# Performance work log

Measured on AMD Instinct MI355X. Metric: run time of the kernel, lower is better.

The kernel has to match this reference:

```python
import jax, jax.numpy as jnp
import numpy as np

B, T, H, W = 2, 4, 32, 32
DINO_DIM, COG_DIM, NUM_HEADS = 768, 1920, 12
HEAD_DIM = DINO_DIM // NUM_HEADS


def _layernorm(x, g, b, eps=1e-5):
    mu = jnp.mean(x, axis=-1, keepdims=True)
    var = jnp.mean(jnp.square(x - mu), axis=-1, keepdims=True)
    return (x - mu) * jax.lax.rsqrt(var + eps) * g + b


def setup_inputs() -> dict:
    key = jax.random.key(0)
    ks = jax.random.split(key, 12)
    s_d = 1.0 / np.sqrt(DINO_DIM)
    s_c = 1.0 / np.sqrt(COG_DIM)
    return {
        "dino_query": jax.random.normal(ks[0], (B, DINO_DIM, H, W), jnp.float32),
        "cogvideo_keys": jax.random.normal(ks[1], (B, T, H, W, COG_DIM), jnp.float32),
        "temporal_weights": jax.random.uniform(ks[2], (T,), jnp.float32),
        "Wq": jax.random.normal(ks[3], (DINO_DIM, DINO_DIM), jnp.float32) * s_d,
        "bq": jnp.zeros((DINO_DIM,), jnp.float32),
        "Wk": jax.random.normal(ks[4], (COG_DIM, DINO_DIM), jnp.float32) * s_c,
        "bk": jnp.zeros((DINO_DIM,), jnp.float32),
        "Wv": jax.random.normal(ks[5], (COG_DIM, DINO_DIM), jnp.float32) * s_c,
        "bv": jnp.zeros((DINO_DIM,), jnp.float32),
        "Wo": jax.random.normal(ks[6], (DINO_DIM, DINO_DIM), jnp.float32) * s_d,
        "bo": jnp.zeros((DINO_DIM,), jnp.float32),
        "gq": jnp.ones((DINO_DIM,), jnp.float32),
        "Bq": jnp.zeros((DINO_DIM,), jnp.float32),
        "gkv": jnp.ones((COG_DIM,), jnp.float32),
        "Bkv": jnp.zeros((COG_DIM,), jnp.float32),
    }


def reference(dino_query, cogvideo_keys, temporal_weights,
              Wq, bq, Wk, bk, Wv, bv, Wo, bo, gq, Bq, gkv, Bkv):
    b, c, h, w = dino_query.shape
    t = cogvideo_keys.shape[1]
    hw, tkv = h * w, t * cogvideo_keys.shape[2] * cogvideo_keys.shape[3]

    # [B,C,H,W] -> [B,H,W,C]; project after LayerNorm
    xq = _layernorm(jnp.transpose(dino_query, (0, 2, 3, 1)), gq, Bq)
    xkv = _layernorm(cogvideo_keys, gkv, Bkv)
    q = xq @ Wq + bq                      # [B,H,W,C]
    k = xkv @ Wk + bk                     # [B,T,Hk,Wk,C]
    v = xkv @ Wv + bv

    q = q.reshape(b, hw, NUM_HEADS, HEAD_DIM).transpose(0, 2, 1, 3)    # [B,nh,HW,hd]
    k = k.reshape(b, tkv, NUM_HEADS, HEAD_DIM).transpose(0, 2, 1, 3)   # [B,nh,TKV,hd]
    v = v.reshape(b, tkv, NUM_HEADS, HEAD_DIM).transpose(0, 2, 1, 3)

    scores = jnp.einsum('bnqd,bnkd->bnqk', q, k) / np.sqrt(HEAD_DIM)   # [B,nh,HW,TKV]
    # per-key temporal weight: each of the T frames contributes HW keys
    w_key = jnp.repeat(temporal_weights, tkv // t)                     # [TKV]
    scores = scores * w_key[None, None, None, :]
    probs = jax.nn.softmax(scores, axis=-1)

    out = jnp.einsum('bnqk,bnkd->bnqd', probs, v)                      # [B,nh,HW,hd]
    out = out.transpose(0, 2, 1, 3).reshape(b, h, w, c)
    out = out @ Wo + bo
    return jnp.transpose(out, (0, 3, 1, 2))                            # [B,C,H,W]
```

## Files before the change

### kernel.cpp

```cpp
#include <hip/hip_runtime.h>
#include <hip/hip_bf16.h>
#include <math.h>

#define BB   2
#define HWl  1024
#define DINO 768
#define COG  1920
#define NHh  12
#define TKV  4096
#define MQ   (BB*HWl)
#define MKV  (BB*TKV)
#define NSPL 4
#define ROWS_PER_SPLIT (BB*NHh*HWl)

typedef __attribute__((ext_vector_type(8))) short bf16x8;
typedef __attribute__((ext_vector_type(4))) float f32x4;

__device__ __forceinline__ unsigned short f2bf_bits(float f) {
    __hip_bfloat16 h = __float2bfloat16(f);
    return *reinterpret_cast<unsigned short*>(&h);
}

__device__ __forceinline__ void glds16(const __hip_bfloat16* g, __hip_bfloat16* l) {
    __builtin_amdgcn_global_load_lds((const __attribute__((address_space(1))) void*)g,
                                     (__attribute__((address_space(3))) void*)l, 16, 0, 0);
}

__global__ __launch_bounds__(256) void prep1(const float* __restrict__ dino,
                                             const float* __restrict__ cog,
                                             const float* __restrict__ gkv, const float* __restrict__ Bkv,
                                             const float* __restrict__ Wq, const float* __restrict__ Wk,
                                             const float* __restrict__ Wv, const float* __restrict__ Wo,
                                             float* __restrict__ xqT,
                                             __hip_bfloat16* __restrict__ xkv,
                                             __hip_bfloat16* WqT, __hip_bfloat16* WkvT, __hip_bfloat16* WoT) {
    int bid = blockIdx.x, tid = threadIdx.x;
    if (bid < 2048) {
        const int W = COG, W4 = W >> 2, NC = 8;
        int row = bid * 4 + (tid >> 6), lane = tid & 63;
        const float4* xr = (const float4*)(cog + (size_t)row * W);
        const float4* g4 = (const float4*)gkv;
        const float4* b4 = (const float4*)Bkv;
        float4 v[NC];
        float s = 0.f, ss = 0.f;
        #pragma unroll
        for (int i = 0; i < NC; ++i) {
            int c = lane + i * 64;
            float4 t = (c < W4) ? xr[c] : (float4){0.f, 0.f, 0.f, 0.f};
            v[i] = t;
            s  += t.x + t.y + t.z + t.w;
            ss += t.x * t.x + t.y * t.y + t.z * t.z + t.w * t.w;
        }
        #pragma unroll
        for (int off = 1; off < 64; off <<= 1) {
            s  += __shfl_xor(s, off);
            ss += __shfl_xor(ss, off);
        }
        float mu = s / W;
        float rstd = rsqrtf(ss / W - mu * mu + 1e-5f);
        ushort4* yr = (ushort4*)(xkv + (size_t)row * W);
        #pragma unroll
        for (int i = 0; i < NC; ++i) {
            int c = lane + i * 64;
            if (c < W4) {
                float4 t = v[i];
                float4 gg = g4[c], bb = b4[c];
                ushort4 o;
                o.x = f2bf_bits((t.x - mu) * rstd * gg.x + bb.x);
                o.y = f2bf_bits((t.y - mu) * rstd * gg.y + bb.y);
                o.z = f2bf_bits((t.z - mu) * rstd * gg.z + bb.z);
                o.w = f2bf_bits((t.w - mu) * rstd * gg.w + bb.w);
                yr[c] = o;
            }
        }
    } else if (bid < 2432) {
        int t = bid - 2048;
        int h0 = (t & 15) * 64;
        int c0 = ((t >> 4) % 12) * 64;
        int b = t / 192;
        __shared__ float T[64][65];
        #pragma unroll
        for (int i = 0; i < 16; ++i) {
            int idx = tid + i * 256;
            int c = idx >> 6, h = idx & 63;
            T[c][h] = dino[((size_t)b * DINO + c0 + c) * HWl + h0 + h];
        }
        __syncthreads();
        #pragma unroll
        for (int i = 0; i < 16; ++i) {
            int idx = tid + i * 256;
            int r = idx >> 6, c = idx & 63;
            xqT[((size_t)b * HWl + h0 + r) * DINO + c0 + c] = T[c][r];
        }
    } else {
        int bid2 = bid - 2432;
        int mid = bid2 / 1440, r = bid2 % 1440;
        int k0 = (r % 60) * 32, n0 = (r / 60) * 32;
        const float* src = (mid == 0) ? Wq : (mid == 1) ? Wk : (mid == 2) ? Wv : Wo;
        __hip_bfloat16* dst;
        int rowoff = 0;
        if (mid == 0) dst = WqT;
        else if (mid == 1) dst = WkvT;
        else if (mid == 2) { dst = WkvT; rowoff = 768; }
        else dst = WoT;
        int K = (mid == 1 || mid == 2) ? COG : DINO;
        if (k0 >= K) return;
        __shared__ float T[32][33];
        #pragma unroll
        for (int i = 0; i < 4; ++i) {
            int idx = tid + i * 256;
            int rr = idx >> 5, c = idx & 31;
            T[rr][c] = src[(size_t)(k0 + rr) * DINO + n0 + c];
        }
        __syncthreads();
        #pragma unroll
        for (int i = 0; i < 4; ++i) {
            int idx = tid + i * 256;
            int rr = idx >> 5, c = idx & 31;
            dst[(size_t)(rowoff + n0 + rr) * K + k0 + c] = __float2bfloat16(T[c][rr]);
        }
    }
}

__global__ __launch_bounds__(256) void prep2(const float* __restrict__ x,
                                             const float* __restrict__ g,
                                             const float* __restrict__ be,
                                             __hip_bfloat16* __restrict__ y) {
    const int W = DINO, NC = 3;
    int row = blockIdx.x * 4 + (threadIdx.x >> 6);
    int lane = threadIdx.x & 63;
    const float4* xr = (const float4*)(x + (size_t)row * W);
    const float4* g4 = (const float4*)g;
    const float4* b4 = (const float4*)be;
    float4 v[NC];
    float s = 0.f, ss = 0.f;
    #pragma unroll
    for (int i = 0; i < NC; ++i) {
        int c = lane + i * 64;
        float4 t = xr[c];
        v[i] = t;
        s  += t.x + t.y + t.z + t.w;
        ss += t.x * t.x + t.y * t.y + t.z * t.z + t.w * t.w;
    }
    #pragma unroll
    for (int off = 1; off < 64; off <<= 1) {
        s  += __shfl_xor(s, off);
        ss += __shfl_xor(ss, off);
    }
    float mu = s / W;
    float rstd = rsqrtf(ss / W - mu * mu + 1e-5f);
    ushort4* yr = (ushort4*)(y + (size_t)row * W);
    #pragma unroll
    for (int i = 0; i < NC; ++i) {
        int c = lane + i * 64;
        float4 t = v[i];
        float4 gg = g4[c], bb = b4[c];
        ushort4 o;
        o.x = f2bf_bits((t.x - mu) * rstd * gg.x + bb.x);
        o.y = f2bf_bits((t.y - mu) * rstd * gg.y + bb.y);
        o.z = f2bf_bits((t.z - mu) * rstd * gg.z + bb.z);
        o.w = f2bf_bits((t.w - mu) * rstd * gg.w + bb.w);
        yr[c] = o;
    }
}

#define VM4 asm volatile("s_waitcnt vmcnt(4)" ::: "memory")
#define VM2 asm volatile("s_waitcnt vmcnt(2)" ::: "memory")
#define VM0 asm volatile("s_waitcnt vmcnt(0)" ::: "memory")

#define STAGE_A(d, h, tau) do { \
    int _o = (aRow + (h) * 64) * Kd + (tau) * 64 + cgo; \
    __hip_bfloat16* _dp = SM + (d) * 32768 + (h) * 8192 + wido; \
    glds16(Ag + _o, _dp); \
    glds16(Ag + _o + 128 * Kd, _dp + 4096); \
} while (0)

#define STAGE_B(d, h, tau) do { \
    int _o = (bRow + (h) * 32) * Kd + (tau) * 64 + cgo; \
    __hip_bfloat16* _dp = SM + (d) * 32768 + 16384 + (h) * 8192 + wido; \
    glds16(Bg + _o, _dp); \
    glds16(Bg + _o + 128 * Kd, _dp + 4096); \
} while (0)

#define LDS_A_FRAG(dst, MH) do { \
    const __hip_bfloat16* _Ab = SM + cur * 32768 + (MH) * 8192 + aoff; \
    _Pragma("unroll") \
    for (int i = 0; i < 4; ++i) { \
        dst[i][0] = *(const bf16x8*)(_Ab + i * 1024 + c0); \
        dst[i][1] = *(const bf16x8*)(_Ab + i * 1024 + c1); \
    } \
} while (0)

#define LDS_B_FRAG(dst, NH) do { \
    const __hip_bfloat16* _Bb = SM + cur * 32768 + 16384 + (NH) * 8192 + boff; \
    _Pragma("unroll") \
    for (int j = 0; j < 2; ++j) { \
        dst[j][0] = *(const bf16x8*)(_Bb + j * 1024 + c0); \
        dst[j][1] = *(const bf16x8*)(_Bb + j * 1024 + c1); \
    } \
} while (0)

#define BARRIER_MFMA(MH, NH, af, bf) do { \
    __builtin_amdgcn_sched_barrier(0); \
    __builtin_amdgcn_s_barrier(); \
    __builtin_amdgcn_sched_barrier(0); \
    __builtin_amdgcn_s_setprio(1); \
    _Pragma("unroll") \
    for (int i = 0; i < 4; ++i) \
        _Pragma("unroll") \
        for (int j = 0; j < 2; ++j) { \
            f32x4 _t = acc[(MH) * 4 + i][(NH) * 2 + j]; \
            _t = __builtin_amdgcn_mfma_f32_16x16x32_bf16(af[i][0], bf[j][0], _t, 0, 0, 0); \
            _t = __builtin_amdgcn_mfma_f32_16x16x32_bf16(af[i][1], bf[j][1], _t, 0, 0, 0); \
            acc[(MH) * 4 + i][(NH) * 2 + j] = _t; \
        } \
    __builtin_amdgcn_s_setprio(0); \
    __builtin_amdgcn_sched_barrier(0); \
} while (0)

__global__ __launch_bounds__(512, 2) void stage1(const __hip_bfloat16* __restrict__ xq,
                                                 const __hip_bfloat16* __restrict__ WqT,
                                                 const float* __restrict__ bq,
                                                 __hip_bfloat16* __restrict__ qb,
                                                 const __hip_bfloat16* __restrict__ xkv,
                                                 const __hip_bfloat16* __restrict__ WkvT,
                                                 const float* __restrict__ bk,
                                                 const float* __restrict__ bv,
                                                 __hip_bfloat16* __restrict__ kb,
                                                 __hip_bfloat16* __restrict__ VT) {
    __shared__ __hip_bfloat16 SM[65536];
    int bid = blockIdx.x;
    int tid = threadIdx.x;
    int wid = tid >> 6, lane = tid & 63;
    int l4 = lane & 15, lq = lane >> 4;
    int wr = wid >> 2, wc = wid & 3;
    int tr = tid >> 3;
    int cgo = ((tid & 7) ^ (tr & 7)) * 8;
    int wido = wid * 512;

    const __hip_bfloat16 *Ag, *Bg;
    int m0, n0, Kd, NT, isQ;
    if (bid < 192) {
        m0 = (bid & 31) * 256; n0 = (bid >> 5) * 256;
        Ag = xkv; Bg = WkvT; Kd = COG; NT = COG / 64; isQ = 0;
    } else {
        int t = bid - 192;
        m0 = (t & 7) * 256; n0 = (t >> 3) * 256;
        Ag = xq; Bg = WqT; Kd = DINO; NT = DINO / 64; isQ = 1;
    }

    const int aRow = m0 + tr;
    const int bRow = n0 + ((tid >> 8) << 6) + (tr & 31);
    const int aoff = (wr * 64 + l4) * 64;
    const int boff = (wc * 32 + l4) * 64;
    const int c0 = ((lq) ^ (l4 & 7)) * 8;
    const int c1 = ((4 + lq) ^ (l4 & 7)) * 8;

    f32x4 acc[8][4];
    #pragma unroll
    for (int i = 0; i < 8; ++i)
        #pragma unroll
        for (int j = 0; j < 4; ++j) acc[i][j] = (f32x4){0.f, 0.f, 0.f, 0.f};

    bf16x8 a0[4][2], a1[4][2], b0[2][2], b1[2][2];

    STAGE_A(0, 0, 0); STAGE_B(0, 0, 0); STAGE_B(0, 1, 0); STAGE_A(0, 1, 0);
    VM0;
    __builtin_amdgcn_s_barrier();

    for (int g = 0; g < NT; ++g) {
        int cur = g & 1, nxt = cur ^ 1;
        bool s1 = (g + 1 < NT);
        LDS_A_FRAG(a0, 0);
        LDS_B_FRAG(b0, 0);
        if (s1) { STAGE_A(nxt, 0, g + 1); VM4; } else { VM2; }
        BARRIER_MFMA(0, 0, a0, b0);
        LDS_B_FRAG(b1, 1);
        if (s1) { STAGE_B(nxt, 0, g + 1); VM4; } else { VM0; }
        BARRIER_MFMA(0, 1, a0, b1);
        LDS_A_FRAG(a1, 1);
        if (s1) { STAGE_B(nxt, 1, g + 1); }
        BARRIER_MFMA(1, 1, a1, b1);
        if (s1) { STAGE_A(nxt, 1, g + 1); VM4; }
        BARRIER_MFMA(1, 0, a1, b0);
    }

    if (isQ) {
        #pragma unroll
        for (int ii = 0; ii < 8; ++ii)
            #pragma unroll
            for (int jj = 0; jj < 4; ++jj) {
                int m = m0 + wr * 128 + (ii >> 2) * 64 + (ii & 3) * 16 + lq * 4;
                int n = n0 + wc * 64 + (jj >> 1) * 32 + (jj & 1) * 16 + l4;
                float bb = bq[n];
                #pragma unroll
                for (int r = 0; r < 4; ++r)
                    qb[(size_t)(m + r) * DINO + n] = __float2bfloat16(acc[ii][jj][r] + bb);
            }
    } else if (n0 < 768) {
        #pragma unroll
        for (int ii = 0; ii < 8; ++ii)
            #pragma unroll
            for (int jj = 0; jj < 4; ++jj) {
                int m = m0 + wr * 128 + (ii >> 2) * 64 + (ii & 3) * 16 + lq * 4;
                int n = n0 + wc * 64 + (jj >> 1) * 32 + (jj & 1) * 16 + l4;
                float bb = bk[n];
                #pragma unroll
                for (int r = 0; r < 4; ++r)
                    kb[(size_t)(m + r) * DINO + n] = __float2bfloat16(acc[ii][jj][r] + bb);
            }
    } else {
        #pragma unroll
        for (int ii = 0; ii < 8; ++ii)
            #pragma unroll
            for (int jj = 0; jj < 4; ++jj) {
                int m = m0 + wr * 128 + (ii >> 2) * 64 + (ii & 3) * 16 + lq * 4;
                int nv = n0 - 768 + wc * 64 + (jj >> 1) * 32 + (jj & 1) * 16 + l4;
                float bb = bv[nv];
                #pragma unroll
                for (int r = 0; r < 4; ++r) {
                    int mm = m + r;
                    VT[((size_t)((mm >> 12) * 768 + nv)) * TKV + (mm & 4095)] =
                        __float2bfloat16(acc[ii][jj][r] + bb);
                }
            }
    }
}

__global__ __launch_bounds__(256) void gemm_o(const __hip_bfloat16* __restrict__ A,
                                              const __hip_bfloat16* __restrict__ Bt,
                                              const float* __restrict__ bias,
                                              float* __restrict__ out) {
    const int K = DINO;
    __shared__ __hip_bfloat16 As[64 * 64];
    __shared__ __hip_bfloat16 Bs[64 * 64];
    int m0 = blockIdx.x * 64, n0 = blockIdx.y * 64;
    int tid = threadIdx.x, w = tid >> 6, lane = tid & 63;
    int l4 = lane & 15, lq = lane >> 4;
    int mq = (w & 1) * 32, nq = (w >> 1) * 32;
    f32x4 acc[2][2];
    #pragma unroll
    for (int i = 0; i < 2; ++i)
        #pragma unroll
        for (int j = 0; j < 2; ++j) acc[i][j] = (f32x4){0.f, 0.f, 0.f, 0.f};

    int rr = tid >> 3;
    int gc = (tid & 7) ^ (rr & 7);
    const __hip_bfloat16* ag = A  + (size_t)(m0 + rr) * K + gc * 8;
    const __hip_bfloat16* bg = Bt + (size_t)(n0 + rr) * K + gc * 8;
    __hip_bfloat16* asl = As + (w * 8) * 64;
    __hip_bfloat16* bsl = Bs + (w * 8) * 64;
    int sws = l4 & 7;

    for (int k0 = 0; k0 < K; k0 += 64) {
        __syncthreads();
        #pragma unroll
        for (int g = 0; g < 2; ++g) {
            glds16(ag + (size_t)(g * 32) * K + k0, asl + g * 32 * 64);
            glds16(bg + (size_t)(g * 32) * K + k0, bsl + g * 32 * 64);
        }
        __syncthreads();
        #pragma unroll
        for (int h = 0; h < 2; ++h) {
            bf16x8 a[2], b[2];
            #pragma unroll
            for (int i = 0; i < 2; ++i)
                a[i] = *(const bf16x8*)(As + (mq + 16 * i + l4) * 64 + (((h * 4 + lq) ^ sws) * 8));
            #pragma unroll
            for (int j = 0; j < 2; ++j)
                b[j] = *(const bf16x8*)(Bs + (nq + 16 * j + l4) * 64 + (((h * 4 + lq) ^ sws) * 8));
            #pragma unroll
            for (int i = 0; i < 2; ++i)
                #pragma unroll
                for (int j = 0; j < 2; ++j)
                    acc[i][j] = __builtin_amdgcn_mfma_f32_16x16x32_bf16(b[j], a[i], acc[i][j], 0, 0, 0);
        }
    }
    #pragma unroll
    for (int i = 0; i < 2; ++i)
        #pragma unroll
        for (int j = 0; j < 2; ++j)
            #pragma unroll
            for (int r = 0; r < 4; ++r) {
                int n = n0 + nq + 16 * j + lq * 4 + r;
                int m = m0 + mq + 16 * i + l4;
                int b = m >> 10, hw = m & 1023;
                out[((size_t)b * DINO + n) * HWl + hw] = acc[i][j][r] + bias[n];
            }
}

__global__ __launch_bounds__(256) void attn4(const __hip_bfloat16* __restrict__ qb,
                                             const __hip_bfloat16* __restrict__ kb,
                                             const __hip_bfloat16* __restrict__ VT,
                                             const float* __restrict__ tw,
                                             __hip_bfloat16* __restrict__ Opart,
                                             float* __restrict__ lpart) {
    int bid = blockIdx.x;
    int g = bid % 96, qc = bid / 96;
    int s = g & 3, bh = g >> 2;
    int head = bh % NHh, b = bh / NHh;
    int tid = threadIdx.x, w = tid >> 6, lane = tid & 63;
    int l4 = lane & 15, lq = lane >> 4;

    __shared__ __hip_bfloat16 Ks[2 * 64 * 64];
    __shared__ __hip_bfloat16 Vs[2 * 64 * 64];
    __shared__ __hip_bfloat16 Ps[4 * 32 * 64];

    const __hip_bfloat16* qbase = qb + (size_t)(b * HWl + qc * 128 + w * 32 + l4) * DINO + head * 64;
    bf16x8 qA0 = *(const bf16x8*)(qbase + lq * 8);
    bf16x8 qA1 = *(const bf16x8*)(qbase + 32 + lq * 8);
    const __hip_bfloat16* qbase2 = qbase + (size_t)16 * DINO;
    bf16x8 qB0 = *(const bf16x8*)(qbase2 + lq * 8);
    bf16x8 qB1 = *(const bf16x8*)(qbase2 + 32 + lq * 8);

    float c = tw[s] * 0.125f * 1.44269504f;
    float l_iA = 0.f, l_iB = 0.f;
    f32x4 oA[4], oB[4];
    #pragma unroll
    for (int j = 0; j < 4; ++j) { oA[j] = (f32x4){0.f,0.f,0.f,0.f}; oB[j] = (f32x4){0.f,0.f,0.f,0.f}; }

    int rowA = w * 16 + (lane >> 3);
    int cg = (lane & 7) ^ ((lane >> 3) & 7);
    const __hip_bfloat16* kg0 = kb + (size_t)(b * TKV + s * 1024 + rowA) * DINO + head * 64 + cg * 8;
    const __hip_bfloat16* kg1 = kg0 + (size_t)8 * DINO;
    const __hip_bfloat16* vg0 = VT + (size_t)(b * 768 + head * 64 + rowA) * TKV + s * 1024 + cg * 8;
    const __hip_bfloat16* vg1 = vg0 + (size_t)8 * TKV;
    int klo0 = (w * 2 + 0) * 512, klo1 = (w * 2 + 1) * 512;

    int sw0 = (lq ^ (l4 & 7)) * 8;
    int sw1 = ((4 + lq) ^ (l4 & 7)) * 8;
    __hip_bfloat16* PsA = Ps + w * 2048 + l4 * 64;
    __hip_bfloat16* PsB = Ps + w * 2048 + (16 + l4) * 64;

    glds16(kg0, Ks + klo0);
    glds16(kg1, Ks + klo1);
    glds16(vg0, Vs + klo0);
    glds16(vg1, Vs + klo1);

    for (int kt = 0; kt < 16; ++kt) {
        int cur = (kt & 1) * 4096;
        __syncthreads();
        if (kt < 15) {
            int nxt = cur ^ 4096;
            glds16(kg0 + (size_t)(kt + 1) * 64 * DINO, Ks + nxt + klo0);
            glds16(kg1 + (size_t)(kt + 1) * 64 * DINO, Ks + nxt + klo1);
            glds16(vg0 + (kt + 1) * 64, Vs + nxt + klo0);
            glds16(vg1 + (kt + 1) * 64, Vs + nxt + klo1);
        }
        const __hip_bfloat16* Kc = Ks + cur;
        const __hip_bfloat16* Vc = Vs + cur;

        f32x4 stA[4], stB[4];
        #pragma unroll
        for (int j = 0; j < 4; ++j) {
            const __hip_bfloat16* kr = Kc + (16 * j + l4) * 64;
            bf16x8 kf0 = *(const bf16x8*)(kr + sw0);
            bf16x8 kf1 = *(const bf16x8*)(kr + sw1);
            f32x4 a = (f32x4){0.f,0.f,0.f,0.f};
            a = __builtin_amdgcn_mfma_f32_16x16x32_bf16(kf0, qA0, a, 0, 0, 0);
            a = __builtin_amdgcn_mfma_f32_16x16x32_bf16(kf1, qA1, a, 0, 0, 0);
            stA[j] = a;
            f32x4 bb = (f32x4){0.f,0.f,0.f,0.f};
            bb = __builtin_amdgcn_mfma_f32_16x16x32_bf16(kf0, qB0, bb, 0, 0, 0);
            bb = __builtin_amdgcn_mfma_f32_16x16x32_bf16(kf1, qB1, bb, 0, 0, 0);
            stB[j] = bb;
        }

        float lsA = 0.f, lsB = 0.f;
        #pragma unroll
        for (int j = 0; j < 4; ++j)
            #pragma unroll
            for (int r = 0; r < 4; ++r) {
                float eA = exp2f(stA[j][r] * c);
                float eB = exp2f(stB[j][r] * c);
                stA[j][r] = eA; lsA += eA;
                stB[j][r] = eB; lsB += eB;
            }
        lsA += __shfl_xor(lsA, 16); lsA += __shfl_xor(lsA, 32);
        lsB += __shfl_xor(lsB, 16); lsB += __shfl_xor(lsB, 32);
        l_iA += lsA; l_iB += lsB;

        #pragma unroll
        for (int j = 0; j < 4; ++j) {
            int off = (((2 * j + (lq >> 1)) ^ (l4 & 7)) << 3) + (lq & 1) * 4;
            ushort4 pA, pB;
            pA.x = f2bf_bits(stA[j][0]); pA.y = f2bf_bits(stA[j][1]);
            pA.z = f2bf_bits(stA[j][2]); pA.w = f2bf_bits(stA[j][3]);
            pB.x = f2bf_bits(stB[j][0]); pB.y = f2bf_bits(stB[j][1]);
            pB.z = f2bf_bits(stB[j][2]); pB.w = f2bf_bits(stB[j][3]);
            *(ushort4*)&PsA[off] = pA;
            *(ushort4*)&PsB[off] = pB;
        }
        bf16x8 paA0 = *(const bf16x8*)(PsA + sw0);
        bf16x8 paA1 = *(const bf16x8*)(PsA + sw1);
        bf16x8 paB0 = *(const bf16x8*)(PsB + sw0);
        bf16x8 paB1 = *(const bf16x8*)(PsB + sw1);

        #pragma unroll
        for (int j = 0; j < 4; ++j) {
            const __hip_bfloat16* vr = Vc + (16 * j + l4) * 64;
            bf16x8 vf0 = *(const bf16x8*)(vr + sw0);
            bf16x8 vf1 = *(const bf16x8*)(vr + sw1);
            oA[j] = __builtin_amdgcn_mfma_f32_16x16x32_bf16(paA0, vf0, oA[j], 0, 0, 0);
            oA[j] = __builtin_amdgcn_mfma_f32_16x16x32_bf16(paA1, vf1, oA[j], 0, 0, 0);
            oB[j] = __builtin_amdgcn_mfma_f32_16x16x32_bf16(paB0, vf0, oB[j], 0, 0, 0);
            oB[j] = __builtin_amdgcn_mfma_f32_16x16x32_bf16(paB1, vf1, oB[j], 0, 0, 0);
        }
    }

    size_t rb = (size_t)s * ROWS_PER_SPLIT + (size_t)(b * NHh + head) * HWl + qc * 128 + w * 32;
    #pragma unroll
    for (int j = 0; j < 4; ++j)
        #pragma unroll
        for (int r = 0; r < 4; ++r) {
            Opart[(rb + lq * 4 + r) * 64 + j * 16 + l4]      = __float2bfloat16(oA[j][r]);
            Opart[(rb + 16 + lq * 4 + r) * 64 + j * 16 + l4] = __float2bfloat16(oB[j][r]);
        }
    if (lq == 0) {
        lpart[rb + l4]      = l_iA;
        lpart[rb + 16 + l4] = l_iB;
    }
}

__global__ void combine(const __hip_bfloat16* __restrict__ Opart, const float* __restrict__ lpart,
                        __hip_bfloat16* __restrict__ attn) {
    int p = blockIdx.x * 4 + (threadIdx.x >> 6);
    int d = threadIdx.x & 63;
    float L = 0.f, O = 0.f;
    #pragma unroll
    for (int s = 0; s < NSPL; ++s) {
        L += lpart[(size_t)s * ROWS_PER_SPLIT + p];
        O += __bfloat162float(Opart[((size_t)s * ROWS_PER_SPLIT + p) * 64 + d]);
    }
    float res = O / L;
    int q = p & 1023;
    int bh = p >> 10;
    int head = bh % NHh, b = bh / NHh;
    attn[((size_t)(b * HWl + q)) * DINO + head * 64 + d] = __float2bfloat16(res);
}

extern "C" void kernel_launch(void* const* d_in, const int* in_sizes, int n_in,
                              void* d_out, int out_size, void* d_ws, size_t ws_size,
                              hipStream_t stream) {
    (void)in_sizes; (void)n_in; (void)out_size; (void)ws_size;
    const float* dino = (const float*)d_in[0];
    const float* cog  = (const float*)d_in[1];
    const float* tw   = (const float*)d_in[2];
    const float* Wq   = (const float*)d_in[3];
    const float* bq   = (const float*)d_in[4];
    const float* Wk   = (const float*)d_in[5];
    const float* bk   = (const float*)d_in[6];
    const float* Wv   = (const float*)d_in[7];
    const float* bv   = (const float*)d_in[8];
    const float* Wo   = (const float*)d_in[9];
    const float* bo   = (const float*)d_in[10];
    const float* gq   = (const float*)d_in[11];
    const float* Bq   = (const float*)d_in[12];
    const float* gkv  = (const float*)d_in[13];
    const float* Bkv  = (const float*)d_in[14];

    char* p = (char*)d_ws;
    float* xqT = (float*)p;                    p += (size_t)MQ * DINO * 4;
    __hip_bfloat16* xq = (__hip_bfloat16*)p;   p += (size_t)MQ * DINO * 2;
    char* alias = p;                           p += (size_t)MKV * COG * 2;
    __hip_bfloat16* xkv = (__hip_bfloat16*)alias;
    __hip_bfloat16* WqT  = (__hip_bfloat16*)p; p += (size_t)DINO * DINO * 2;
    __hip_bfloat16* WkvT = (__hip_bfloat16*)p; p += (size_t)1536 * COG * 2;
    __hip_bfloat16* WoT  = (__hip_bfloat16*)p; p += (size_t)DINO * DINO * 2;
    __hip_bfloat16* qb   = (__hip_bfloat16*)p; p += (size_t)MQ  * DINO * 2;
    __hip_bfloat16* kb   = (__hip_bfloat16*)p; p += (size_t)MKV * DINO * 2;
    __hip_bfloat16* VT   = (__hip_bfloat16*)p; p += (size_t)MKV * DINO * 2;
    __hip_bfloat16* attnb = (__hip_bfloat16*)p; p += (size_t)MQ * DINO * 2;
    __hip_bfloat16* Opart = (__hip_bfloat16*)alias;
    float* lpart = (float*)(alias + (size_t)NSPL * ROWS_PER_SPLIT * 64 * 2);

    prep1<<<8192, 256, 0, stream>>>(dino, cog, gkv, Bkv,
                                    Wq, Wk, Wv, Wo, xqT, xkv, WqT, WkvT, WoT);
    prep2<<<MQ / 4, 256, 0, stream>>>(xqT, gq, Bq, xq);
    stage1<<<216, 512, 0, stream>>>(xq, WqT, bq, qb, xkv, WkvT, bk, bv, kb, VT);
    attn4<<<BB * NHh * 8 * NSPL, 256, 0, stream>>>(qb, kb, VT, tw, Opart, lpart);
    combine<<<ROWS_PER_SPLIT / 4, 256, 0, stream>>>(Opart, lpart, attnb);
    gemm_o<<<dim3(32, 12), 256, 0, stream>>>(attnb, WoT, bo, (float*)d_out);
}
```

Measured before the change: 255.5 us.

## Merge stage1 GEMM loop into two barrier phases and swizzle KV block mapping

The stage1 projection GEMM main loop is cut from four barrier-separated MFMA phases per K-tile to two. Each phase now covers one A half against both B halves. The next tile's A0/B0/B1 loads are issued together with relaxed vmcnt waits, and the prologue no longer drains all loads. This halves the workgroup barriers and should leave more global loads in flight, at the cost of changing the overlap between LDS reads, prefetch and MFMA. The KV-projection block index is also remapped so that consecutive blocks share B (weight) column tiles across nearby M tiles, for better L2 reuse.

```diff
diff --git a/kernel.cpp b/kernel.cpp
--- a/kernel.cpp
+++ b/kernel.cpp
@@ -164,7 +164,7 @@
     }
 }
 
-#define VM4 asm volatile("s_waitcnt vmcnt(4)" ::: "memory")
+#define VM6 asm volatile("s_waitcnt vmcnt(6)" ::: "memory")
 #define VM2 asm volatile("s_waitcnt vmcnt(2)" ::: "memory")
 #define VM0 asm volatile("s_waitcnt vmcnt(0)" ::: "memory")
 
@@ -200,7 +200,7 @@
     } \
 } while (0)
 
-#define BARRIER_MFMA(MH, NH, af, bf) do { \
+#define PHASE_MFMA(MH, af) do { \
     __builtin_amdgcn_sched_barrier(0); \
     __builtin_amdgcn_s_barrier(); \
     __builtin_amdgcn_sched_barrier(0); \
@@ -209,13 +209,21 @@
     for (int i = 0; i < 4; ++i) \
         _Pragma("unroll") \
         for (int j = 0; j < 2; ++j) { \
-            f32x4 _t = acc[(MH) * 4 + i][(NH) * 2 + j]; \
-            _t = __builtin_amdgcn_mfma_f32_16x16x32_bf16(af[i][0], bf[j][0], _t, 0, 0, 0); \
-            _t = __builtin_amdgcn_mfma_f32_16x16x32_bf16(af[i][1], bf[j][1], _t, 0, 0, 0); \
-            acc[(MH) * 4 + i][(NH) * 2 + j] = _t; \
+            f32x4 _t = acc[(MH) * 4 + i][j]; \
+            _t = __builtin_amdgcn_mfma_f32_16x16x32_bf16(af[i][0], b0[j][0], _t, 0, 0, 0); \
+            _t = __builtin_amdgcn_mfma_f32_16x16x32_bf16(af[i][1], b0[j][1], _t, 0, 0, 0); \
+            acc[(MH) * 4 + i][j] = _t; \
+        } \
+    _Pragma("unroll") \
+    for (int i = 0; i < 4; ++i) \
+        _Pragma("unroll") \
+        for (int j = 0; j < 2; ++j) { \
+            f32x4 _t = acc[(MH) * 4 + i][2 + j]; \
+            _t = __builtin_amdgcn_mfma_f32_16x16x32_bf16(af[i][0], b1[j][0], _t, 0, 0, 0); \
+            _t = __builtin_amdgcn_mfma_f32_16x16x32_bf16(af[i][1], b1[j][1], _t, 0, 0, 0); \
+            acc[(MH) * 4 + i][2 + j] = _t; \
         } \
     __builtin_amdgcn_s_setprio(0); \
-    __builtin_amdgcn_sched_barrier(0); \
 } while (0)
 
 __global__ __launch_bounds__(512, 2) void stage1(const __hip_bfloat16* __restrict__ xq,
@@ -241,7 +249,8 @@
     const __hip_bfloat16 *Ag, *Bg;
     int m0, n0, Kd, NT, isQ;
     if (bid < 192) {
-        m0 = (bid & 31) * 256; n0 = (bid >> 5) * 256;
+        int x = bid & 7, i = bid >> 3;
+        m0 = (x * 4 + (i & 3)) * 256; n0 = (i >> 2) * 256;
         Ag = xkv; Bg = WkvT; Kd = COG; NT = COG / 64; isQ = 0;
     } else {
         int t = bid - 192;
@@ -265,7 +274,7 @@
     bf16x8 a0[4][2], a1[4][2], b0[2][2], b1[2][2];
 
     STAGE_A(0, 0, 0); STAGE_B(0, 0, 0); STAGE_B(0, 1, 0); STAGE_A(0, 1, 0);
-    VM0;
+    VM2;
     __builtin_amdgcn_s_barrier();
 
     for (int g = 0; g < NT; ++g) {
@@ -273,16 +282,13 @@
         bool s1 = (g + 1 < NT);
         LDS_A_FRAG(a0, 0);
         LDS_B_FRAG(b0, 0);
-        if (s1) { STAGE_A(nxt, 0, g + 1); VM4; } else { VM2; }
-        BARRIER_MFMA(0, 0, a0, b0);
         LDS_B_FRAG(b1, 1);
-        if (s1) { STAGE_B(nxt, 0, g + 1); VM4; } else { VM0; }
-        BARRIER_MFMA(0, 1, a0, b1);
+        if (s1) { STAGE_A(nxt, 0, g + 1); STAGE_B(nxt, 0, g + 1); STAGE_B(nxt, 1, g + 1); VM6; }
+        else VM0;
+        PHASE_MFMA(0, a0);
         LDS_A_FRAG(a1, 1);
-        if (s1) { STAGE_B(nxt, 1, g + 1); }
-        BARRIER_MFMA(1, 1, a1, b1);
-        if (s1) { STAGE_A(nxt, 1, g + 1); VM4; }
-        BARRIER_MFMA(1, 0, a1, b0);
+        if (s1) { STAGE_A(nxt, 1, g + 1); VM2; }
+        PHASE_MFMA(1, a1);
     }
 
     if (isQ) {
```

New measurement: 255.5 us. Within noise of the previous version (-0.0%).
